# Optimization experiments

Measured on AMD Instinct MI355X. Metric: run time of the kernel, lower is better.

## Reference

```python
import jax, jax.numpy as jnp
import numpy as np

HUGE = jnp.float32(1e31)   # ops.HUGE_INT
EPS = 1e-20
B, AN = 1024, 256
D = 256            # emb_dim
HD = 512           # history_dim
AD = 2 * D         # action_dim
NE, NR = 100000, 400


def setup_inputs() -> dict:
    key = jax.random.key(0)
    ks = jax.random.split(key, 12)
    e = jax.random.randint(ks[0], (B,), 0, NE)
    q = jax.random.randint(ks[1], (B,), 0, NR)
    hstate = jax.random.normal(ks[2], (B, HD), dtype=jnp.float32)
    r_space = jax.random.randint(ks[3], (B, AN), 0, NR)
    e_space = jax.random.randint(ks[4], (B, AN), 0, NE)
    # binary action mask; guarantee at least one valid action per row
    action_mask = (jax.random.uniform(ks[5], (B, AN)) > 0.2).astype(jnp.float32)
    action_mask = action_mask.at[:, 0].set(1.0)
    entity_emb = jax.random.normal(ks[6], (NE, D), dtype=jnp.float32) * 0.02
    relation_emb = jax.random.normal(ks[7], (NR, D), dtype=jnp.float32) * 0.02
    W1 = jax.random.normal(ks[8], (2 * D + HD, AD), dtype=jnp.float32) * (1.0 / np.sqrt(2 * D + HD))
    b1 = jnp.zeros((AD,), dtype=jnp.float32)
    W2 = jax.random.normal(ks[9], (AD, AD), dtype=jnp.float32) * (1.0 / np.sqrt(AD))
    b2 = jnp.zeros((AD,), dtype=jnp.float32)
    return {"e": e, "q": q, "hstate": hstate, "r_space": r_space,
            "e_space": e_space, "action_mask": action_mask,
            "entity_emb": entity_emb, "relation_emb": relation_emb,
            "W1": W1, "b1": b1, "W2": W2, "b2": b2}


def reference(e, q, hstate, r_space, e_space, action_mask,
              entity_emb, relation_emb, W1, b1, W2, b2):
    Q = relation_emb[q]                       # [B, D]
    E = entity_emb[e]                         # [B, D]
    X = jnp.concatenate([E, hstate, Q], axis=-1)          # [B, 2D+HD]
    X = jax.nn.relu(X @ W1 + b1)                          # [B, AD]
    X2 = X @ W2 + b2                                      # [B, AD]
    # action embeddings: [rel_emb[r]; ent_emb[e]] per padded action slot
    A = jnp.concatenate([relation_emb[r_space], entity_emb[e_space]], axis=-1)  # [B, AN, AD]
    scores = jnp.einsum('bad,bd->ba', A, X2) - (1.0 - action_mask) * HUGE      # [B, AN]
    action_dist = jax.nn.softmax(scores, axis=-1)
    entropy = -jnp.sum(action_dist * jnp.log(jnp.clip(action_dist, EPS)), axis=-1)  # [B]
    return action_dist, entropy
```

## Files before the change

kernel.cpp:

```cpp
#include <hip/hip_runtime.h>
#include <math.h>

#define NB   1024
#define NACT 256
#define DIM  256
#define HDIM 512
#define ADIM 512
#define KTOT 1024
#define NE   100000
#define NR   400
#define CONVB 1024

typedef __attribute__((ext_vector_type(8))) short bf16x8;
typedef __attribute__((ext_vector_type(4))) float f32x4;

__device__ __forceinline__ unsigned short f2bf(float f) {
    unsigned int u = __float_as_uint(f);
    u += 0x7FFF + ((u >> 16) & 1);
    return (unsigned short)(u >> 16);
}
__device__ __forceinline__ float bf2f(unsigned short u) {
    return __uint_as_float(((unsigned int)u) << 32 - 16);
}

__global__ __launch_bounds__(256) void prep_transpose(
    const float* __restrict__ W1, const float* __restrict__ W2,
    ushort* __restrict__ W1T, ushort* __restrict__ W2T)
{
    __shared__ float t[64][68];
    const int z = blockIdx.z;
    if (z && blockIdx.x >= 8) return;
    const int Kd = z ? 512 : 1024;
    const float* in = z ? W2 : W1;
    ushort* out = z ? W2T : W1T;
    const int k0 = blockIdx.x * 64, n0 = blockIdx.y * 64;
    const int tid = threadIdx.x;
    const int kr = tid >> 2, c = tid & 3;
    #pragma unroll
    for (int j = 0; j < 4; ++j) {
        const float4 v = *(const float4*)(in + (size_t)(k0 + kr) * ADIM + n0 + c * 16 + j * 4);
        *(float4*)&t[kr][c * 16 + j * 4] = v;
    }
    __syncthreads();
    const int nr = tid >> 2;
    ushort tmp[16];
    #pragma unroll
    for (int kk = 0; kk < 16; ++kk) tmp[kk] = f2bf(t[c * 16 + kk][nr]);
    *(uint4*)(out + (size_t)(n0 + nr) * Kd + k0 + c * 16)     = *(uint4*)&tmp[0];
    *(uint4*)(out + (size_t)(n0 + nr) * Kd + k0 + c * 16 + 8) = *(uint4*)&tmp[8];
}

__global__ __launch_bounds__(256) void mega_conv_gemm1(
    const float* __restrict__ ent, const float* __restrict__ rel,
    const float* __restrict__ hstate,
    const int* __restrict__ e, const int* __restrict__ q,
    const ushort* __restrict__ W1T, const float* __restrict__ b1,
    ushort* __restrict__ entbf, ushort* __restrict__ relbf,
    ushort* __restrict__ Hbf)
{
    const int blk = blockIdx.x, tid = threadIdx.x;
    __shared__ __align__(16) ushort Als[64][40];
    __shared__ __align__(16) ushort Bls[64][40];

    if (blk < CONVB) {
        const float4* src = (const float4*)ent;
        ushort4* dst = (ushort4*)entbf;
        const int start = blk * 6250;
        for (int j = start + tid; j < start + 6250; j += 256) {
            const float4 v = src[j];
            ushort4 o = {f2bf(v.x), f2bf(v.y), f2bf(v.z), f2bf(v.w)};
            dst[j] = o;
        }
        if (blk < 100) {
            const int j = blk * 256 + tid;
            const float4 v = ((const float4*)rel)[j];
            ushort4 o = {f2bf(v.x), f2bf(v.y), f2bf(v.z), f2bf(v.w)};
            ((ushort4*)relbf)[j] = o;
        }
        return;
    }

    const int g  = blk - CONVB;
    const int n0 = (g & 7) * 64;
    const int m0 = (g >> 3) * 64;
    const int wave = tid >> 6, lane = tid & 63;
    const int qq   = lane >> 4, l15 = lane & 15;
    const int sm   = tid >> 2, sc = tid & 3;
    const int kofs = sc * 8;

    const int row   = m0 + sm;
    const float* rowE = ent + (size_t)e[row] * DIM;
    const float* rowH = hstate + (size_t)row * HDIM - DIM;
    const float* rowQ = rel + (size_t)q[row] * DIM - (DIM + HDIM);
    const uint4* gb = (const uint4*)(W1T + (size_t)(n0 + sm) * KTOT) + sc;

    f32x4 acc[4];
    #pragma unroll
    for (int mt = 0; mt < 4; ++mt) acc[mt] = (f32x4){0.f, 0.f, 0.f, 0.f};

    float4 pa0 = *(const float4*)(rowE + kofs);
    float4 pa1 = *(const float4*)(rowE + kofs + 4);
    uint4  pb  = gb[0];

    for (int it = 0; it < KTOT / 32; ++it) {
        ushort t8[8];
        t8[0] = f2bf(pa0.x); t8[1] = f2bf(pa0.y); t8[2] = f2bf(pa0.z); t8[3] = f2bf(pa0.w);
        t8[4] = f2bf(pa1.x); t8[5] = f2bf(pa1.y); t8[6] = f2bf(pa1.z); t8[7] = f2bf(pa1.w);
        *(uint4*)&Als[sm][sc * 8] = *(uint4*)t8;
        *(uint4*)&Bls[sm][sc * 8] = pb;
        __syncthreads();
        if (it + 1 < KTOT / 32) {
            const int kg = (it + 1) * 32 + kofs;
            const float* src = (kg < DIM) ? rowE : ((kg < DIM + HDIM) ? rowH : rowQ);
            pa0 = *(const float4*)(src + kg);
            pa1 = *(const float4*)(src + kg + 4);
            pb  = gb[(it + 1) * 4];
        }
        const bf16x8 bfrag = *(const bf16x8*)&Bls[wave * 16 + l15][qq * 8];
        #pragma unroll
        for (int mt = 0; mt < 4; ++mt) {
            const bf16x8 afrag = *(const bf16x8*)&Als[mt * 16 + l15][qq * 8];
            acc[mt] = __builtin_amdgcn_mfma_f32_16x16x32_bf16(afrag, bfrag, acc[mt], 0, 0, 0);
        }
        __syncthreads();
    }
    const int n = n0 + wave * 16 + l15;
    const float bv = b1[n];
    #pragma unroll
    for (int mt = 0; mt < 4; ++mt)
        #pragma unroll
        for (int r = 0; r < 4; ++r) {
            const int m = m0 + mt * 16 + qq * 4 + r;
            Hbf[(size_t)m * ADIM + n] = f2bf(fmaxf(acc[mt][r] + bv, 0.0f));
        }
}

__global__ __launch_bounds__(256) void gemm2_mfma(
    const ushort* __restrict__ A, const ushort* __restrict__ Bt,
    const float* __restrict__ bias, float* __restrict__ Cf)
{
    __shared__ __align__(16) ushort Als[64][40];
    __shared__ __align__(16) ushort Bls[64][40];
    const int tid  = threadIdx.x;
    const int n0   = blockIdx.x * 64;
    const int m0   = blockIdx.y * 64;
    const int wave = tid >> 6, lane = tid & 63;
    const int qq   = lane >> 4, l15 = lane & 15;
    const int sm   = tid >> 2, sc = tid & 3;

    const uint4* ga = (const uint4*)(A  + (size_t)(m0 + sm) * ADIM) + sc;
    const uint4* gb = (const uint4*)(Bt + (size_t)(n0 + sm) * ADIM) + sc;

    f32x4 acc[4];
    #pragma unroll
    for (int mt = 0; mt < 4; ++mt) acc[mt] = (f32x4){0.f, 0.f, 0.f, 0.f};

    uint4 pa = ga[0], pb = gb[0];
    for (int it = 0; it < ADIM / 32; ++it) {
        *(uint4*)&Als[sm][sc * 8] = pa;
        *(uint4*)&Bls[sm][sc * 8] = pb;
        __syncthreads();
        if (it + 1 < ADIM / 32) {
            pa = ga[(it + 1) * 4];
            pb = gb[(it + 1) * 4];
        }
        const bf16x8 bfrag = *(const bf16x8*)&Bls[wave * 16 + l15][qq * 8];
        #pragma unroll
        for (int mt = 0; mt < 4; ++mt) {
            const bf16x8 afrag = *(const bf16x8*)&Als[mt * 16 + l15][qq * 8];
            acc[mt] = __builtin_amdgcn_mfma_f32_16x16x32_bf16(afrag, bfrag, acc[mt], 0, 0, 0);
        }
        __syncthreads();
    }
    const int n = n0 + wave * 16 + l15;
    const float bv = bias[n];
    #pragma unroll
    for (int mt = 0; mt < 4; ++mt)
        #pragma unroll
        for (int r = 0; r < 4; ++r) {
            const int m = m0 + mt * 16 + qq * 4 + r;
            Cf[(size_t)m * ADIM + n] = acc[mt][r] + bv;
        }
}

__global__ __launch_bounds__(512) void scores_kernel(
    const int* __restrict__ r_space, const int* __restrict__ e_space,
    const float* __restrict__ amask,
    const ushort* __restrict__ relbf, const ushort* __restrict__ entbf,
    const float* __restrict__ X2,
    float* __restrict__ dist_out, float* __restrict__ ent_out)
{
    const int b    = blockIdx.x;
    const int tid  = threadIdx.x;
    const int wave = tid >> 6;
    const int lane = tid & 63;

    __shared__ float xs[ADIM];
    __shared__ float sc[NACT];
    __shared__ int   ridx[NACT];
    __shared__ int   eidx[NACT];
    __shared__ float red1[8], red2[8], red3[8];

    if (tid < NACT) ridx[tid] = r_space[(size_t)b * NACT + tid];
    else            eidx[tid - NACT] = e_space[(size_t)b * NACT + tid - NACT];
    if (tid < ADIM / 4)
        ((float4*)xs)[tid] = ((const float4*)(X2 + (size_t)b * ADIM))[tid];
    __syncthreads();

    const float4 xr = ((const float4*)xs)[lane];
    const float4 xe = ((const float4*)(xs + DIM))[lane];

    const int abase = wave * 32;
    for (int a0 = abase; a0 < abase + 32; a0 += 8) {
        ushort4 rv[8], ev[8];
        #pragma unroll
        for (int i = 0; i < 8; ++i) {
            rv[i] = ((const ushort4*)relbf)[(size_t)ridx[a0 + i] * (DIM / 4) + lane];
            ev[i] = ((const ushort4*)entbf)[(size_t)eidx[a0 + i] * (DIM / 4) + lane];
        }
        float p[8];
        #pragma unroll
        for (int i = 0; i < 8; ++i) {
            p[i] = bf2f(rv[i].x) * xr.x + bf2f(rv[i].y) * xr.y
                 + bf2f(rv[i].z) * xr.z + bf2f(rv[i].w) * xr.w
                 + bf2f(ev[i].x) * xe.x + bf2f(ev[i].y) * xe.y
                 + bf2f(ev[i].z) * xe.z + bf2f(ev[i].w) * xe.w;
        }
        #pragma unroll
        for (int off = 32; off; off >>= 1) {
            #pragma unroll
            for (int i = 0; i < 8; ++i) p[i] += __shfl_xor(p[i], off);
        }
        float out = p[0];
        #pragma unroll
        for (int i = 1; i < 8; ++i) out = (lane == i) ? p[i] : out;
        if (lane < 8) sc[a0 + lane] = out;
    }
    __syncthreads();

    float s = -3.0e38f;
    if (tid < NACT) {
        const float m = amask[(size_t)b * NACT + tid];
        s = sc[tid] - (1.0f - m) * 1e31f;
    }

    float mx = s;
    #pragma unroll
    for (int off = 32; off; off >>= 1) mx = fmaxf(mx, __shfl_xor(mx, off));
    if (lane == 0) red1[wave] = mx;
    __syncthreads();
    mx = red1[0];
    #pragma unroll
    for (int w = 1; w < 8; ++w) mx = fmaxf(mx, red1[w]);

    const float ex = (tid < NACT) ? expf(s - mx) : 0.0f;
    float sum = ex;
    #pragma unroll
    for (int off = 32; off; off >>= 1) sum += __shfl_xor(sum, off);
    if (lane == 0) red2[wave] = sum;
    __syncthreads();
    sum = ((red2[0] + red2[1]) + (red2[2] + red2[3]))
        + ((red2[4] + red2[5]) + (red2[6] + red2[7]));

    const float d = ex / sum;
    if (tid < NACT) dist_out[(size_t)b * NACT + tid] = d;

    float t = (tid < NACT) ? d * logf(fmaxf(d, 1e-20f)) : 0.0f;
    #pragma unroll
    for (int off = 32; off; off >>= 1) t += __shfl_xor(t, off);
    if (lane == 0) red3[wave] = t;
    __syncthreads();
    if (tid == 0)
        ent_out[b] = -(((red3[0] + red3[1]) + (red3[2] + red3[3]))
                     + ((red3[4] + red3[5]) + (red3[6] + red3[7])));
}

extern "C" void kernel_launch(void* const* d_in, const int* in_sizes, int n_in,
                              void* d_out, int out_size, void* d_ws, size_t ws_size,
                              hipStream_t stream) {
    const int*   e       = (const int*)d_in[0];
    const int*   q       = (const int*)d_in[1];
    const float* hstate  = (const float*)d_in[2];
    const int*   r_space = (const int*)d_in[3];
    const int*   e_space = (const int*)d_in[4];
    const float* amask   = (const float*)d_in[5];
    const float* ent     = (const float*)d_in[6];
    const float* rel     = (const float*)d_in[7];
    const float* W1      = (const float*)d_in[8];
    const float* b1      = (const float*)d_in[9];
    const float* W2      = (const float*)d_in[10];
    const float* b2      = (const float*)d_in[11];

    ushort* W1T   = (ushort*)d_ws;
    ushort* W2T   = W1T   + (size_t)ADIM * KTOT;
    ushort* Hbf   = W2T   + (size_t)ADIM * ADIM;
    ushort* entbf = Hbf   + (size_t)NB * ADIM;
    ushort* relbf = entbf + (size_t)NE * DIM;
    float*  X2    = (float*)(relbf + (size_t)NR * DIM);
    float*  dist  = (float*)d_out;
    float*  entr  = dist + (size_t)NB * NACT;

    prep_transpose<<<dim3(16, 8, 2), 256, 0, stream>>>(W1, W2, W1T, W2T);
    mega_conv_gemm1<<<CONVB + 128, 256, 0, stream>>>(
        ent, rel, hstate, e, q, W1T, b1, entbf, relbf, Hbf);
    gemm2_mfma<<<dim3(ADIM / 64, NB / 64), 256, 0, stream>>>(Hbf, W2T, b2, X2);
    scores_kernel<<<NB, 512, 0, stream>>>(
        r_space, e_space, amask, relbf, entbf, X2, dist, entr);
}
```

Measured before the change: 227.2 us.

## Precompute relation scores via GEMM against all relations and reorder conv/gemm1 blocks

Because there are only 400 relations, the relation half of each action score is computed once per batch row as a dense X2_rel × relation_emb^T GEMM into a [B,448] table, and the scores kernel just looks it up instead of gathering 256-dim relation rows per action. The scores kernel now gathers only entity rows, 16 actions per iteration. The GEMM1 blocks are placed before the conversion blocks so they are scheduled first, and the conversion loop is unrolled by four. This adds a kernel launch and rounds X2 to bf16 for the relation part, which slightly changes numerics.

```diff
diff --git a/kernel.cpp b/kernel.cpp
--- a/kernel.cpp
+++ b/kernel.cpp
@@ -9,7 +9,8 @@
 #define KTOT 1024
 #define NE   100000
 #define NR   400
-#define CONVB 1024
+#define NRP  448
+#define G1B  128
 
 typedef __attribute__((ext_vector_type(8))) short bf16x8;
 typedef __attribute__((ext_vector_type(4))) float f32x4;
@@ -20,7 +21,11 @@
     return (unsigned short)(u >> 16);
 }
 __device__ __forceinline__ float bf2f(unsigned short u) {
-    return __uint_as_float(((unsigned int)u) << 32 - 16);
+    return __uint_as_float(((unsigned int)u) << 16);
+}
+__device__ __forceinline__ ushort4 cvt4(float4 v) {
+    ushort4 o = {f2bf(v.x), f2bf(v.y), f2bf(v.z), f2bf(v.w)};
+    return o;
 }
 
 __global__ __launch_bounds__(256) void prep_transpose(
@@ -62,25 +67,32 @@
     __shared__ __align__(16) ushort Als[64][40];
     __shared__ __align__(16) ushort Bls[64][40];
 
-    if (blk < CONVB) {
+    if (blk >= G1B) {
+        const int cb = blk - G1B;
         const float4* src = (const float4*)ent;
         ushort4* dst = (ushort4*)entbf;
-        const int start = blk * 6250;
-        for (int j = start + tid; j < start + 6250; j += 256) {
-            const float4 v = src[j];
-            ushort4 o = {f2bf(v.x), f2bf(v.y), f2bf(v.z), f2bf(v.w)};
-            dst[j] = o;
-        }
-        if (blk < 100) {
-            const int j = blk * 256 + tid;
-            const float4 v = ((const float4*)rel)[j];
-            ushort4 o = {f2bf(v.x), f2bf(v.y), f2bf(v.z), f2bf(v.w)};
-            ((ushort4*)relbf)[j] = o;
+        const int start = cb * 6250;
+        const int end = start + 6250;
+        int j = start + tid;
+        for (; j + 768 < end; j += 1024) {
+            const float4 v0 = src[j];
+            const float4 v1 = src[j + 256];
+            const float4 v2 = src[j + 512];
+            const float4 v3 = src[j + 768];
+            dst[j]       = cvt4(v0);
+            dst[j + 256] = cvt4(v1);
+            dst[j + 512] = cvt4(v2);
+            dst[j + 768] = cvt4(v3);
+        }
+        for (; j < end; j += 256) dst[j] = cvt4(src[j]);
+        if (cb < 100) {
+            const int k = cb * 256 + tid;
+            ((ushort4*)relbf)[k] = cvt4(((const float4*)rel)[k]);
         }
         return;
     }
 
-    const int g  = blk - CONVB;
+    const int g  = blk;
     const int n0 = (g & 7) * 64;
     const int m0 = (g >> 3) * 64;
     const int wave = tid >> 6, lane = tid & 63;
@@ -137,7 +149,8 @@
 
 __global__ __launch_bounds__(256) void gemm2_mfma(
     const ushort* __restrict__ A, const ushort* __restrict__ Bt,
-    const float* __restrict__ bias, float* __restrict__ Cf)
+    const float* __restrict__ bias, float* __restrict__ Cf,
+    ushort* __restrict__ X2rbf)
 {
     __shared__ __align__(16) ushort Als[64][40];
     __shared__ __align__(16) ushort Bls[64][40];
@@ -174,19 +187,72 @@
     }
     const int n = n0 + wave * 16 + l15;
     const float bv = bias[n];
+    const bool lowhalf = (n0 < 256);
     #pragma unroll
     for (int mt = 0; mt < 4; ++mt)
         #pragma unroll
         for (int r = 0; r < 4; ++r) {
             const int m = m0 + mt * 16 + qq * 4 + r;
-            Cf[(size_t)m * ADIM + n] = acc[mt][r] + bv;
-        }
+            const float v = acc[mt][r] + bv;
+            Cf[(size_t)m * ADIM + n] = v;
+            if (lowhalf) X2rbf[(size_t)m * DIM + n] = f2bf(v);
+        }
+}
+
+__global__ __launch_bounds__(256) void gemm_rel(
+    const ushort* __restrict__ A, const ushort* __restrict__ Bt,
+    float* __restrict__ R)
+{
+    __shared__ __align__(16) ushort Als[64][40];
+    __shared__ __align__(16) ushort Bls[64][40];
+    const int tid  = threadIdx.x;
+    const int n0   = blockIdx.x * 64;
+    const int m0   = blockIdx.y * 64;
+    const int wave = tid >> 6, lane = tid & 63;
+    const int qq   = lane >> 4, l15 = lane & 15;
+    const int sm   = tid >> 2, sc = tid & 3;
+
+    const int brow = (n0 + sm < NR) ? (n0 + sm) : (NR - 1);
+    const uint4* ga = (const uint4*)(A  + (size_t)(m0 + sm) * DIM) + sc;
+    const uint4* gb = (const uint4*)(Bt + (size_t)brow * DIM) + sc;
+
+    f32x4 acc[4];
+    #pragma unroll
+    for (int mt = 0; mt < 4; ++mt) acc[mt] = (f32x4){0.f, 0.f, 0.f, 0.f};
+
+    uint4 pa = ga[0], pb = gb[0];
+    for (int it = 0; it < DIM / 32; ++it) {
+        *(uint4*)&Als[sm][sc * 8] = pa;
+        *(uint4*)&Bls[sm][sc * 8] = pb;
+        __syncthreads();
+        if (it + 1 < DIM / 32) {
+            pa = ga[(it + 1) * 4];
+            pb = gb[(it + 1) * 4];
+        }
+        const bf16x8 bfrag = *(const bf16x8*)&Bls[wave * 16 + l15][qq * 8];
+        #pragma unroll
+        for (int mt = 0; mt < 4; ++mt) {
+            const bf16x8 afrag = *(const bf16x8*)&Als[mt * 16 + l15][qq * 8];
+            acc[mt] = __builtin_amdgcn_mfma_f32_16x16x32_bf16(afrag, bfrag, acc[mt], 0, 0, 0);
+        }
+        __syncthreads();
+    }
+    const int n = n0 + wave * 16 + l15;
+    if (n < NR) {
+        #pragma unroll
+        for (int mt = 0; mt < 4; ++mt)
+            #pragma unroll
+            for (int r = 0; r < 4; ++r) {
+                const int m = m0 + mt * 16 + qq * 4 + r;
+                R[(size_t)m * NRP + n] = acc[mt][r];
+            }
+    }
 }
 
 __global__ __launch_bounds__(512) void scores_kernel(
     const int* __restrict__ r_space, const int* __restrict__ e_space,
     const float* __restrict__ amask,
-    const ushort* __restrict__ relbf, const ushort* __restrict__ entbf,
+    const ushort* __restrict__ entbf, const float* __restrict__ R,
     const float* __restrict__ X2,
     float* __restrict__ dist_out, float* __restrict__ ent_out)
 {
@@ -207,34 +273,31 @@
         ((float4*)xs)[tid] = ((const float4*)(X2 + (size_t)b * ADIM))[tid];
     __syncthreads();
 
-    const float4 xr = ((const float4*)xs)[lane];
     const float4 xe = ((const float4*)(xs + DIM))[lane];
+    const float* R_row = R + (size_t)b * NRP;
 
     const int abase = wave * 32;
-    for (int a0 = abase; a0 < abase + 32; a0 += 8) {
-        ushort4 rv[8], ev[8];
-        #pragma unroll
-        for (int i = 0; i < 8; ++i) {
-            rv[i] = ((const ushort4*)relbf)[(size_t)ridx[a0 + i] * (DIM / 4) + lane];
+    for (int a0 = abase; a0 < abase + 32; a0 += 16) {
+        const float rsc = (lane < 16) ? R_row[ridx[a0 + lane]] : 0.0f;
+        ushort4 ev[16];
+        #pragma unroll
+        for (int i = 0; i < 16; ++i)
             ev[i] = ((const ushort4*)entbf)[(size_t)eidx[a0 + i] * (DIM / 4) + lane];
-        }
-        float p[8];
-        #pragma unroll
-        for (int i = 0; i < 8; ++i) {
-            p[i] = bf2f(rv[i].x) * xr.x + bf2f(rv[i].y) * xr.y
-                 + bf2f(rv[i].z) * xr.z + bf2f(rv[i].w) * xr.w
-                 + bf2f(ev[i].x) * xe.x + bf2f(ev[i].y) * xe.y
+        float p[16];
+        #pragma unroll
+        for (int i = 0; i < 16; ++i) {
+            p[i] = bf2f(ev[i].x) * xe.x + bf2f(ev[i].y) * xe.y
                  + bf2f(ev[i].z) * xe.z + bf2f(ev[i].w) * xe.w;
         }
         #pragma unroll
         for (int off = 32; off; off >>= 1) {
             #pragma unroll
-            for (int i = 0; i < 8; ++i) p[i] += __shfl_xor(p[i], off);
+            for (int i = 0; i < 16; ++i) p[i] += __shfl_xor(p[i], off);
         }
         float out = p[0];
         #pragma unroll
-        for (int i = 1; i < 8; ++i) out = (lane == i) ? p[i] : out;
-        if (lane < 8) sc[a0 + lane] = out;
+        for (int i = 1; i < 16; ++i) out = (lane == i) ? p[i] : out;
+        if (lane < 16) sc[a0 + lane] = out + rsc;
     }
     __syncthreads();
 
@@ -297,13 +360,16 @@
     ushort* entbf = Hbf   + (size_t)NB * ADIM;
     ushort* relbf = entbf + (size_t)NE * DIM;
     float*  X2    = (float*)(relbf + (size_t)NR * DIM);
+    ushort* X2rbf = (ushort*)(X2 + (size_t)NB * ADIM);
+    float*  Rtab  = (float*)(X2rbf + (size_t)NB * DIM);
     float*  dist  = (float*)d_out;
     float*  entr  = dist + (size_t)NB * NACT;
 
     prep_transpose<<<dim3(16, 8, 2), 256, 0, stream>>>(W1, W2, W1T, W2T);
-    mega_conv_gemm1<<<CONVB + 128, 256, 0, stream>>>(
+    mega_conv_gemm1<<<G1B + 1024, 256, 0, stream>>>(
         ent, rel, hstate, e, q, W1T, b1, entbf, relbf, Hbf);
-    gemm2_mfma<<<dim3(ADIM / 64, NB / 64), 256, 0, stream>>>(Hbf, W2T, b2, X2);
+    gemm2_mfma<<<dim3(ADIM / 64, NB / 64), 256, 0, stream>>>(Hbf, W2T, b2, X2, X2rbf);
+    gemm_rel<<<dim3(NRP / 64, NB / 64), 256, 0, stream>>>(X2rbf, relbf, Rtab);
     scores_kernel<<<NB, 512, 0, stream>>>(
-        r_space, e_space, amask, relbf, entbf, X2, dist, entr);
-}
+        r_space, e_space, amask, entbf, Rtab, X2, dist, entr);
+}
```

Result: slower. 234.8 us (+3.3%).
